# Optimization experiments

Measured on AMD Instinct MI355X. Metric: run time of the kernel, lower is better.

Reference implementation:

```python
import jax, jax.numpy as jnp
import numpy as np

TOP_K = 2


def setup_inputs() -> dict:
    key = jax.random.key(0)
    ks = jax.random.split(key, 10)
    D, F, E = 1024, 4096, 8
    s = 0.02  # realistic init scale, keeps activations stable
    return {
        "x": jax.random.normal(ks[0], (2, 4096, D), dtype=jnp.float32),
        "gate_w": jax.random.normal(ks[1], (E, D), dtype=jnp.float32) * s,
        "w1": jax.random.normal(ks[2], (E, F, D), dtype=jnp.float32) * s,
        "b1": jax.random.normal(ks[3], (E, F), dtype=jnp.float32) * s,
        "w2": jax.random.normal(ks[4], (E, D, F), dtype=jnp.float32) * s,
        "b2": jax.random.normal(ks[5], (E, D), dtype=jnp.float32) * s,
        "sw1": jax.random.normal(ks[6], (F, D), dtype=jnp.float32) * s,
        "sb1": jax.random.normal(ks[7], (F,), dtype=jnp.float32) * s,
        "sw2": jax.random.normal(ks[8], (D, F), dtype=jnp.float32) * s,
        "sb2": jax.random.normal(ks[9], (D,), dtype=jnp.float32) * s,
    }


def _ffn(x, w1, b1, w2, b2):
    # GELU(x @ W1^T + b1) @ W2^T + b2 ; torch F.gelu default = exact (erf)
    h = jax.nn.gelu(x @ w1.T + b1, approximate=False)
    return h @ w2.T + b2


def reference(x, gate_w, w1, b1, w2, b2, sw1, sb1, sw2, sb2):
    B, S, D = x.shape
    E = gate_w.shape[0]
    xt = x.reshape(-1, D)  # [T, D]

    # MoEGate: linear -> softmax -> top-k (weights not renormalized)
    scores = jax.nn.softmax(xt @ gate_w.T, axis=-1)  # [T, E]
    topk_w, topk_idx = jax.lax.top_k(scores, TOP_K)  # [T, K]

    # moe_infer: per-expert FFN, combine with top-k gate weights.
    # Reference form: dense per-expert compute, masked combine (combine sum is
    # permutation-invariant so top-k ordering does not matter).
    out = jnp.zeros_like(xt)
    for e in range(E):
        we = jnp.sum(jnp.where(topk_idx == e, topk_w, 0.0), axis=-1)  # [T]
        out = out + we[:, None] * _ffn(xt, w1[e], b1[e], w2[e], b2[e])

    # shared expert applied to the identity input
    out = out + _ffn(xt, sw1, sb1, sw2, sb2)
    return out.reshape(B, S, D)
```

## Files before the change

### kernel.cpp

```cpp
#include <hip/hip_runtime.h>
#include <hip/hip_bf16.h>

typedef __bf16 bf16_t;
typedef __bf16 bf16x4 __attribute__((ext_vector_type(4)));
typedef __bf16 bf16x8 __attribute__((ext_vector_type(8)));
typedef float  f32x4  __attribute__((ext_vector_type(4)));

static constexpr int TT = 8192;
static constexpr int DD = 1024;
static constexpr int FF = 4096;
static constexpr int NSLOT = 2 * TT;

#define R_COUNTS 0
#define R_OFFSET 8
#define R_TSTART 17
#define R_TOTAL  34
#define R_INTS   40

#define GLL(g, l) __builtin_amdgcn_global_load_lds( \
    (__attribute__((address_space(1))) void*)(g), \
    (__attribute__((address_space(3))) void*)(l), 16, 0, 0)

__device__ __forceinline__ float fast_gelu(float v) {
  float t = -1.5957691216f * v - 0.0713548162f * (v * v * v);
  return v / (1.f + __expf(t));
}

__global__ __launch_bounds__(256) void cvt_all(const float* __restrict__ w1,
                                               const float* __restrict__ w2,
                                               const float* __restrict__ sw1,
                                               const float* __restrict__ sw2,
                                               bf16_t* __restrict__ dst) {
  size_t i = (size_t)blockIdx.x * 256 + threadIdx.x;
  const float* src;
  size_t off;
  if (i < 4194304)      { src = w1;  off = i; }
  else if (i < 8388608) { src = w2;  off = i - 4194304; }
  else if (i < 8912896) { src = sw1; off = i - 8388608; }
  else                  { src = sw2; off = i - 8912896; }
  const float4* s = reinterpret_cast<const float4*>(src) + off * 2;
  float4 a = s[0], b = s[1];
  bf16x8 v;
  v[0] = (bf16_t)a.x; v[1] = (bf16_t)a.y; v[2] = (bf16_t)a.z; v[3] = (bf16_t)a.w;
  v[4] = (bf16_t)b.x; v[5] = (bf16_t)b.y; v[6] = (bf16_t)b.z; v[7] = (bf16_t)b.w;
  *reinterpret_cast<bf16x8*>(dst + i * 8) = v;
}

__global__ __launch_bounds__(256) void gate_kernel(const float* __restrict__ x,
                                                   const float* __restrict__ gw,
                                                   float* __restrict__ topkw,
                                                   int* __restrict__ slote,
                                                   bf16_t* __restrict__ xb) {
  int wid = threadIdx.x >> 6, lane = threadIdx.x & 63;
  int t = blockIdx.x * 4 + wid;
  const float4* xv = reinterpret_cast<const float4*>(x + (size_t)t * DD) + lane * 4;
  const float4* gv = reinterpret_cast<const float4*>(gw);
  float acc[8];
  float4 xs[4];
#pragma unroll
  for (int e = 0; e < 8; ++e) acc[e] = 0.f;
#pragma unroll
  for (int i = 0; i < 4; ++i) {
    float4 xi = xv[i];
    xs[i] = xi;
#pragma unroll
    for (int e = 0; e < 8; ++e) {
      float4 g = gv[e * 256 + lane * 4 + i];
      acc[e] += xi.x * g.x + xi.y * g.y + xi.z * g.z + xi.w * g.w;
    }
  }
  {
    bf16x8 lo, hi;
    lo[0]=(bf16_t)xs[0].x; lo[1]=(bf16_t)xs[0].y; lo[2]=(bf16_t)xs[0].z; lo[3]=(bf16_t)xs[0].w;
    lo[4]=(bf16_t)xs[1].x; lo[5]=(bf16_t)xs[1].y; lo[6]=(bf16_t)xs[1].z; lo[7]=(bf16_t)xs[1].w;
    hi[0]=(bf16_t)xs[2].x; hi[1]=(bf16_t)xs[2].y; hi[2]=(bf16_t)xs[2].z; hi[3]=(bf16_t)xs[2].w;
    hi[4]=(bf16_t)xs[3].x; hi[5]=(bf16_t)xs[3].y; hi[6]=(bf16_t)xs[3].z; hi[7]=(bf16_t)xs[3].w;
    bf16_t* d = xb + (size_t)t * DD + lane * 16;
    *reinterpret_cast<bf16x8*>(d) = lo;
    *reinterpret_cast<bf16x8*>(d + 8) = hi;
  }
#pragma unroll
  for (int e = 0; e < 8; ++e)
    for (int off = 32; off; off >>= 1) acc[e] += __shfl_xor(acc[e], off, 64);
  if (lane == 0) {
    float m = acc[0];
#pragma unroll
    for (int e = 1; e < 8; ++e) m = fmaxf(m, acc[e]);
    float p[8], s = 0.f;
#pragma unroll
    for (int e = 0; e < 8; ++e) { p[e] = expf(acc[e] - m); s += p[e]; }
    float inv = 1.f / s;
#pragma unroll
    for (int e = 0; e < 8; ++e) p[e] *= inv;
    int e1 = 0; float b1v = p[0];
#pragma unroll
    for (int e = 1; e < 8; ++e) if (p[e] > b1v) { b1v = p[e]; e1 = e; }
    int e2 = -1; float b2v = -1.f;
#pragma unroll
    for (int e = 0; e < 8; ++e) if (e != e1 && p[e] > b2v) { b2v = p[e]; e2 = e; }
    topkw[2 * t] = b1v;  topkw[2 * t + 1] = b2v;
    slote[2 * t] = e1;   slote[2 * t + 1] = e2;
  }
}

__global__ __launch_bounds__(256) void route_kernel(const int* __restrict__ slote,
                                                    int* __restrict__ routing,
                                                    int* __restrict__ perm,
                                                    int* __restrict__ pos) {
  __shared__ int sl[16384];
  __shared__ int red[256];
  __shared__ int wtot[4];
  const int e = blockIdx.x;
  const int t = threadIdx.x;
  const int lane = t & 63, wid = t >> 6;

  for (int i = t; i < NSLOT; i += 256) sl[i] = slote[i];
  __syncthreads();

  int cnt[8];
#pragma unroll
  for (int ee = 0; ee < 8; ++ee) cnt[ee] = 0;
  for (int i = t; i < NSLOT; i += 256) ++cnt[sl[i]];

  int tot[8];
#pragma unroll
  for (int ee = 0; ee < 8; ++ee) {
    red[t] = cnt[ee];
    __syncthreads();
    for (int s = 128; s; s >>= 1) {
      if (t < s) red[t] += red[t + s];
      __syncthreads();
    }
    tot[ee] = red[0];
    __syncthreads();
  }

  int offarr[9], tstart[9];
  {
    int off = 0, tts = 0;
#pragma unroll
    for (int ee = 0; ee < 8; ++ee) {
      offarr[ee] = off; tstart[ee] = tts;
      off += tot[ee]; tts += (tot[ee] + 127) >> 7;
    }
    offarr[8] = off; tstart[8] = tts;
  }
  if (e == 0 && t == 0) {
#pragma unroll
    for (int ee = 0; ee < 8; ++ee) routing[R_COUNTS + ee] = tot[ee];
#pragma unroll
    for (int ee = 0; ee < 9; ++ee) {
      routing[R_OFFSET + ee] = offarr[ee];
      routing[R_TSTART + ee] = tstart[ee];
    }
    routing[R_TOTAL] = tstart[8];
  }

  int running = offarr[e];
  for (int base = 0; base < NSLOT; base += 256) {
    int s = base + t;
    bool m = (sl[s] == e);
    unsigned long long mask = __ballot(m);
    int wrank = __popcll(mask & ((1ull << lane) - 1ull));
    if (lane == 0) wtot[wid] = __popcll(mask);
    __syncthreads();
    int wpre = 0;
#pragma unroll
    for (int w = 0; w < 4; ++w) if (w < wid) wpre += wtot[w];
    int totb = wtot[0] + wtot[1] + wtot[2] + wtot[3];
    if (m) {
      int pp = running + wpre + wrank;
      perm[pp] = s;
      pos[s] = pp;
    }
    running += totb;
    __syncthreads();
  }
}

template <int MODE>
__global__ __launch_bounds__(256, 4) void gemm_kernel(
    const bf16_t* __restrict__ A, const bf16_t* __restrict__ Bw,
    const float* __restrict__ bias, bf16_t* __restrict__ Hout,
    float* __restrict__ out, const int* __restrict__ routing,
    const int* __restrict__ perm, const float* __restrict__ topkw,
    const int* __restrict__ pos, const bf16_t* __restrict__ slotb) {
  constexpr bool EXPERT = (MODE < 2);
  constexpr int K = (MODE == 0 || MODE == 2) ? 1024 : 4096;
  constexpr int NTOT = (MODE == 0 || MODE == 2) ? 4096 : 1024;
  constexpr int NT = NTOT / 128;
  constexpr int NKT = K / 64;
  constexpr int OUTD = (MODE == 0 || MODE == 2) ? FF : DD;

  __shared__ __align__(16) bf16_t lds[16384];

  const int t = threadIdx.x;
  const int lane = t & 63;
  const int wid = t >> 6;
  const int wm = wid >> 1;
  const int wn = wid & 1;

  const int nwg = gridDim.x;
  const int q = nwg >> 3, r = nwg & 7;
  const int xcd = blockIdx.x & 7, bi = blockIdx.x >> 3;
  const int swz = (xcd < r ? xcd * (q + 1) : r * (q + 1) + (xcd - r) * q) + bi;
  const int mt = swz / NT;
  const int nt = swz & (NT - 1);

  int row0, valid, eidx = 0;
  if constexpr (EXPERT) {
    if (mt >= routing[R_TOTAL]) return;
    int e = 0;
    while (e < 7 && routing[R_TSTART + e + 1] <= mt) ++e;
    eidx = e;
    int lm = mt - routing[R_TSTART + e];
    row0 = routing[R_OFFSET + e] + lm * 128;
    valid = min(128, routing[R_COUNTS + e] - lm * 128);
  } else {
    row0 = mt * 128;
    valid = 128;
  }

  const bf16_t* Bexp = Bw + (EXPERT ? (size_t)eidx * NTOT * K : 0);
  const float* biasp = bias + (EXPERT ? eidx * NTOT : 0);

  const int sub = t >> 3;
  const int lc = (t & 7) ^ (sub & 7);
  const bf16_t* aS[4];
  const bf16_t* bS[4];
#pragma unroll
  for (int i = 0; i < 4; ++i) {
    int lr = sub + i * 32;
    int gr;
    if constexpr (MODE == 0) {
      gr = perm[row0 + min(lr, valid - 1)] >> 1;
    } else if constexpr (MODE == 1) {
      gr = row0 + min(lr, valid - 1);
    } else {
      gr = row0 + lr;
    }
    aS[i] = A + (size_t)gr * K + lc * 8;
    bS[i] = Bexp + (size_t)(nt * 128 + lr) * K + lc * 8;
  }
  bf16_t* const aD = lds + (sub << 6) + ((t & 7) << 3);
  bf16_t* const bD = aD + 8192;

  const int l15 = lane & 15, lq = lane >> 4;

  f32x4 acc[4][4];
#pragma unroll
  for (int m = 0; m < 4; ++m)
#pragma unroll
    for (int n = 0; n < 4; ++n) acc[m][n] = f32x4{0.f, 0.f, 0.f, 0.f};

  for (int kt = 0; kt < NKT; ++kt) {
    const size_t kof = (size_t)kt * 64;
#pragma unroll
    for (int i = 0; i < 4; ++i) {
      GLL(aS[i] + kof, aD + i * 2048);
      GLL(bS[i] + kof, bD + i * 2048);
    }
    __syncthreads();

#pragma unroll
    for (int kk = 0; kk < 2; ++kk) {
      bf16x8 af[4], bfr[4];
#pragma unroll
      for (int m = 0; m < 4; ++m) {
        int ra = wm * 64 + m * 16 + l15;
        int ph = (kk * 4 + lq) ^ (ra & 7);
        af[m] = *reinterpret_cast<const bf16x8*>(&lds[ra * 64 + ph * 8]);
      }
#pragma unroll
      for (int n = 0; n < 4; ++n) {
        int rb = wn * 64 + n * 16 + l15;
        int ph = (kk * 4 + lq) ^ (rb & 7);
        bfr[n] = *reinterpret_cast<const bf16x8*>(&lds[8192 + rb * 64 + ph * 8]);
      }
      __builtin_amdgcn_s_setprio(1);
#pragma unroll
      for (int m = 0; m < 4; ++m)
#pragma unroll
        for (int n = 0; n < 4; ++n)
          acc[m][n] = __builtin_amdgcn_mfma_f32_16x16x32_bf16(af[m], bfr[n], acc[m][n], 0, 0, 0);
      __builtin_amdgcn_s_setprio(0);
    }
    __syncthreads();
  }

  float bc[4];
#pragma unroll
  for (int n = 0; n < 4; ++n) bc[n] = biasp[nt * 128 + wn * 64 + n * 16 + l15];

  if constexpr (MODE != 3) {
    bf16_t* scr = lds;
#pragma unroll
    for (int h = 0; h < 2; ++h) {
      __syncthreads();
      if (wm == h) {
        float wsl[4][4];
        if constexpr (MODE == 1) {
#pragma unroll
          for (int m = 0; m < 4; ++m)
#pragma unroll
            for (int rr = 0; rr < 4; ++rr) {
              int lr = h * 64 + m * 16 + lq * 4 + rr;
              wsl[m][rr] = topkw[perm[row0 + min(lr, valid - 1)]];
            }
        }
#pragma unroll
        for (int m = 0; m < 4; ++m)
#pragma unroll
          for (int n = 0; n < 4; ++n)
#pragma unroll
            for (int rr = 0; rr < 4; ++rr) {
              float v = acc[m][n][rr] + bc[n];
              float o;
              if constexpr (MODE == 1) o = wsl[m][rr] * v;
              else                     o = fast_gelu(v);
              scr[(m * 16 + lq * 4 + rr) * 128 + wn * 64 + n * 16 + l15] = (bf16_t)o;
            }
      }
      __syncthreads();
#pragma unroll
      for (int i = 0; i < 4; ++i) {
        int c = t + i * 256;
        int rowp = c >> 4, cc = c & 15;
        int lr = h * 64 + rowp;
        if (lr < valid) {
          bf16x8 v8 = *reinterpret_cast<const bf16x8*>(&scr[rowp * 128 + cc * 8]);
          *reinterpret_cast<bf16x8*>(&Hout[(size_t)(row0 + lr) * OUTD + nt * 128 + cc * 8]) = v8;
        }
      }
    }
  } else {
    float* scr = reinterpret_cast<float*>(lds);
#pragma unroll
    for (int h = 0; h < 2; ++h) {
      __syncthreads();
      if (wm == h) {
#pragma unroll
        for (int m = 0; m < 4; ++m)
#pragma unroll
          for (int n = 0; n < 4; ++n)
#pragma unroll
            for (int rr = 0; rr < 4; ++rr)
              scr[(m * 16 + lq * 4 + rr) * 128 + wn * 64 + n * 16 + l15] = acc[m][n][rr] + bc[n];
      }
      __syncthreads();
#pragma unroll
      for (int i = 0; i < 8; ++i) {
        int c = t + i * 256;
        int rowp = c >> 5, cc = c & 31;
        int lr = h * 64 + rowp;
        int gp = row0 + lr;
        int p0 = pos[2 * gp], p1 = pos[2 * gp + 1];
        float4 v4 = *reinterpret_cast<const float4*>(&scr[rowp * 128 + cc * 4]);
        bf16x4 s0 = *reinterpret_cast<const bf16x4*>(&slotb[(size_t)p0 * DD + nt * 128 + cc * 4]);
        bf16x4 s1 = *reinterpret_cast<const bf16x4*>(&slotb[(size_t)p1 * DD + nt * 128 + cc * 4]);
        v4.x += (float)s0[0] + (float)s1[0];
        v4.y += (float)s0[1] + (float)s1[1];
        v4.z += (float)s0[2] + (float)s1[2];
        v4.w += (float)s0[3] + (float)s1[3];
        *reinterpret_cast<float4*>(&out[(size_t)gp * OUTD + nt * 128 + cc * 4]) = v4;
      }
    }
  }
}

extern "C" void kernel_launch(void* const* d_in, const int* in_sizes, int n_in,
                              void* d_out, int out_size, void* d_ws, size_t ws_size,
                              hipStream_t stream) {
  const float* x   = (const float*)d_in[0];
  const float* gw  = (const float*)d_in[1];
  const float* w1  = (const float*)d_in[2];
  const float* b1  = (const float*)d_in[3];
  const float* w2  = (const float*)d_in[4];
  const float* b2  = (const float*)d_in[5];
  const float* sw1 = (const float*)d_in[6];
  const float* sb1 = (const float*)d_in[7];
  const float* sw2 = (const float*)d_in[8];
  const float* sb2 = (const float*)d_in[9];
  float* out = (float*)d_out;

  char* ws = (char*)d_ws;
  bf16_t* xb    = (bf16_t*)(ws);
  bf16_t* w1b   = (bf16_t*)(ws + ((size_t)16 << 20));
  bf16_t* w2b   = (bf16_t*)(ws + ((size_t)80 << 20));
  bf16_t* sw1b  = (bf16_t*)(ws + ((size_t)144 << 20));
  bf16_t* sw2b  = (bf16_t*)(ws + ((size_t)152 << 20));
  bf16_t* Hbuf  = (bf16_t*)(ws + ((size_t)160 << 20));
  bf16_t* slotb = (bf16_t*)(ws + ((size_t)16 << 20));
  float*  topkw = (float*)(ws + ((size_t)288 << 20));
  int*    slote = (int*)(ws + ((size_t)288 << 20) + 65536);
  int*    perm  = (int*)(ws + ((size_t)288 << 20) + 2 * 65536);
  int*    pos   = (int*)(ws + ((size_t)288 << 20) + 3 * 65536);
  int*    routing = (int*)(ws + ((size_t)288 << 20) + 4 * 65536);

  cvt_all<<<9437184 / 256, 256, 0, stream>>>(w1, w2, sw1, sw2, w1b);

  gate_kernel<<<TT / 4, 256, 0, stream>>>(x, gw, topkw, slote, xb);
  route_kernel<<<8, 256, 0, stream>>>(slote, routing, perm, pos);

  gemm_kernel<0><<<136 * 32, 256, 0, stream>>>(xb, w1b, b1, Hbuf, nullptr, routing, perm, nullptr, nullptr, nullptr);
  gemm_kernel<1><<<136 * 8, 256, 0, stream>>>(Hbuf, w2b, b2, slotb, nullptr, routing, perm, topkw, nullptr, nullptr);
  gemm_kernel<2><<<64 * 32, 256, 0, stream>>>(xb, sw1b, sb1, Hbuf, nullptr, routing, perm, nullptr, nullptr, nullptr);
  gemm_kernel<3><<<64 * 8, 256, 0, stream>>>(Hbuf, sw2b, sb2, nullptr, out, routing, perm, nullptr, pos, slotb);
}
```

Measured before the change: 692.9 us.

## Merge weight conversion with gating and co-schedule expert GEMM2 with shared GEMM1

Weight fp32→bf16 conversion and the gate kernel now run as one launch, with the block index choosing the role. When the workspace is large enough, the expert down-projection GEMM and the shared-expert up-projection GEMM run as one grid. The shared hidden activations go to a separate buffer so the two GEMMs do not overwrite each other's inputs. This removes launch gaps and tail underutilization between independent stages, and it depends on the workspace size to enable the merged path.

```diff
diff --git a/kernel.cpp b/kernel.cpp
--- a/kernel.cpp
+++ b/kernel.cpp
@@ -10,6 +10,10 @@
 static constexpr int DD = 1024;
 static constexpr int FF = 4096;
 static constexpr int NSLOT = 2 * TT;
+static constexpr int GATE_BLKS = TT / 4;
+static constexpr int CVT_BLKS = 9437184 / 256;
+static constexpr int EG2_BLKS = 136 * 8;
+static constexpr int SG1_BLKS = 64 * 32;
 
 #define R_COUNTS 0
 #define R_OFFSET 8
@@ -26,31 +30,32 @@
   return v / (1.f + __expf(t));
 }
 
-__global__ __launch_bounds__(256) void cvt_all(const float* __restrict__ w1,
-                                               const float* __restrict__ w2,
-                                               const float* __restrict__ sw1,
-                                               const float* __restrict__ sw2,
-                                               bf16_t* __restrict__ dst) {
-  size_t i = (size_t)blockIdx.x * 256 + threadIdx.x;
-  const float* src;
-  size_t off;
-  if (i < 4194304)      { src = w1;  off = i; }
-  else if (i < 8388608) { src = w2;  off = i - 4194304; }
-  else if (i < 8912896) { src = sw1; off = i - 8388608; }
-  else                  { src = sw2; off = i - 8912896; }
-  const float4* s = reinterpret_cast<const float4*>(src) + off * 2;
-  float4 a = s[0], b = s[1];
-  bf16x8 v;
-  v[0] = (bf16_t)a.x; v[1] = (bf16_t)a.y; v[2] = (bf16_t)a.z; v[3] = (bf16_t)a.w;
-  v[4] = (bf16_t)b.x; v[5] = (bf16_t)b.y; v[6] = (bf16_t)b.z; v[7] = (bf16_t)b.w;
-  *reinterpret_cast<bf16x8*>(dst + i * 8) = v;
-}
-
-__global__ __launch_bounds__(256) void gate_kernel(const float* __restrict__ x,
+__global__ __launch_bounds__(256) void prep_kernel(const float* __restrict__ x,
                                                    const float* __restrict__ gw,
                                                    float* __restrict__ topkw,
                                                    int* __restrict__ slote,
-                                                   bf16_t* __restrict__ xb) {
+                                                   bf16_t* __restrict__ xb,
+                                                   const float* __restrict__ w1,
+                                                   const float* __restrict__ w2,
+                                                   const float* __restrict__ sw1,
+                                                   const float* __restrict__ sw2,
+                                                   bf16_t* __restrict__ wdst) {
+  if ((int)blockIdx.x >= GATE_BLKS) {
+    size_t i = (size_t)(blockIdx.x - GATE_BLKS) * 256 + threadIdx.x;
+    const float* src;
+    size_t off;
+    if (i < 4194304)      { src = w1;  off = i; }
+    else if (i < 8388608) { src = w2;  off = i - 4194304; }
+    else if (i < 8912896) { src = sw1; off = i - 8388608; }
+    else                  { src = sw2; off = i - 8912896; }
+    const float4* s = reinterpret_cast<const float4*>(src) + off * 2;
+    float4 a = s[0], b = s[1];
+    bf16x8 v;
+    v[0] = (bf16_t)a.x; v[1] = (bf16_t)a.y; v[2] = (bf16_t)a.z; v[3] = (bf16_t)a.w;
+    v[4] = (bf16_t)b.x; v[5] = (bf16_t)b.y; v[6] = (bf16_t)b.z; v[7] = (bf16_t)b.w;
+    *reinterpret_cast<bf16x8*>(wdst + i * 8) = v;
+    return;
+  }
   int wid = threadIdx.x >> 6, lane = threadIdx.x & 63;
   int t = blockIdx.x * 4 + wid;
   const float4* xv = reinterpret_cast<const float4*>(x + (size_t)t * DD) + lane * 4;
@@ -179,7 +184,8 @@
 }
 
 template <int MODE>
-__global__ __launch_bounds__(256, 4) void gemm_kernel(
+__device__ __forceinline__ void gemm_body(
+    int vbid, int nwg, bf16_t* lds,
     const bf16_t* __restrict__ A, const bf16_t* __restrict__ Bw,
     const float* __restrict__ bias, bf16_t* __restrict__ Hout,
     float* __restrict__ out, const int* __restrict__ routing,
@@ -192,17 +198,14 @@
   constexpr int NKT = K / 64;
   constexpr int OUTD = (MODE == 0 || MODE == 2) ? FF : DD;
 
-  __shared__ __align__(16) bf16_t lds[16384];
-
   const int t = threadIdx.x;
   const int lane = t & 63;
   const int wid = t >> 6;
   const int wm = wid >> 1;
   const int wn = wid & 1;
 
-  const int nwg = gridDim.x;
   const int q = nwg >> 3, r = nwg & 7;
-  const int xcd = blockIdx.x & 7, bi = blockIdx.x >> 3;
+  const int xcd = vbid & 7, bi = vbid >> 3;
   const int swz = (xcd < r ? xcd * (q + 1) : r * (q + 1) + (xcd - r) * q) + bi;
   const int mt = swz / NT;
   const int nt = swz & (NT - 1);
@@ -368,6 +371,35 @@
   }
 }
 
+template <int MODE>
+__global__ __launch_bounds__(256, 4) void gemm_single(
+    const bf16_t* __restrict__ A, const bf16_t* __restrict__ Bw,
+    const float* __restrict__ bias, bf16_t* __restrict__ Hout,
+    float* __restrict__ out, const int* __restrict__ routing,
+    const int* __restrict__ perm, const float* __restrict__ topkw,
+    const int* __restrict__ pos, const bf16_t* __restrict__ slotb) {
+  __shared__ __align__(16) bf16_t lds[16384];
+  gemm_body<MODE>(blockIdx.x, gridDim.x, lds, A, Bw, bias, Hout, out,
+                  routing, perm, topkw, pos, slotb);
+}
+
+__global__ __launch_bounds__(256, 4) void gemm_eg2_sg1(
+    const bf16_t* __restrict__ Hexp, const bf16_t* __restrict__ w2b,
+    const float* __restrict__ b2, bf16_t* __restrict__ slotb,
+    const bf16_t* __restrict__ xb, const bf16_t* __restrict__ sw1b,
+    const float* __restrict__ sb1, bf16_t* __restrict__ sHbuf,
+    const int* __restrict__ routing, const int* __restrict__ perm,
+    const float* __restrict__ topkw) {
+  __shared__ __align__(16) bf16_t lds[16384];
+  if ((int)blockIdx.x < EG2_BLKS) {
+    gemm_body<1>(blockIdx.x, EG2_BLKS, lds, Hexp, w2b, b2, slotb, nullptr,
+                 routing, perm, topkw, nullptr, nullptr);
+  } else {
+    gemm_body<2>(blockIdx.x - EG2_BLKS, SG1_BLKS, lds, xb, sw1b, sb1, sHbuf,
+                 nullptr, routing, perm, nullptr, nullptr, nullptr);
+  }
+}
+
 extern "C" void kernel_launch(void* const* d_in, const int* in_sizes, int n_in,
                               void* d_out, int out_size, void* d_ws, size_t ws_size,
                               hipStream_t stream) {
@@ -397,13 +429,25 @@
   int*    pos   = (int*)(ws + ((size_t)288 << 20) + 3 * 65536);
   int*    routing = (int*)(ws + ((size_t)288 << 20) + 4 * 65536);
 
-  cvt_all<<<9437184 / 256, 256, 0, stream>>>(w1, w2, sw1, sw2, w1b);
-
-  gate_kernel<<<TT / 4, 256, 0, stream>>>(x, gw, topkw, slote, xb);
+  const bool bigws = ws_size >= ((size_t)368 << 20);
+  bf16_t* sHbuf = bigws ? (bf16_t*)(ws + ((size_t)304 << 20)) : Hbuf;
+
+  prep_kernel<<<GATE_BLKS + CVT_BLKS, 256, 0, stream>>>(x, gw, topkw, slote, xb,
+                                                        w1, w2, sw1, sw2, w1b);
   route_kernel<<<8, 256, 0, stream>>>(slote, routing, perm, pos);
 
-  gemm_kernel<0><<<136 * 32, 256, 0, stream>>>(xb, w1b, b1, Hbuf, nullptr, routing, perm, nullptr, nullptr, nullptr);
-  gemm_kernel<1><<<136 * 8, 256, 0, stream>>>(Hbuf, w2b, b2, slotb, nullptr, routing, perm, topkw, nullptr, nullptr);
-  gemm_kernel<2><<<64 * 32, 256, 0, stream>>>(xb, sw1b, sb1, Hbuf, nullptr, routing, perm, nullptr, nullptr, nullptr);
-  gemm_kernel<3><<<64 * 8, 256, 0, stream>>>(Hbuf, sw2b, sb2, nullptr, out, routing, perm, nullptr, pos, slotb);
-}
+  gemm_single<0><<<136 * 32, 256, 0, stream>>>(xb, w1b, b1, Hbuf, nullptr, routing,
+                                               perm, nullptr, nullptr, nullptr);
+  if (bigws) {
+    gemm_eg2_sg1<<<EG2_BLKS + SG1_BLKS, 256, 0, stream>>>(Hbuf, w2b, b2, slotb,
+                                                          xb, sw1b, sb1, sHbuf,
+                                                          routing, perm, topkw);
+  } else {
+    gemm_single<1><<<EG2_BLKS, 256, 0, stream>>>(Hbuf, w2b, b2, slotb, nullptr,
+                                                 routing, perm, topkw, nullptr, nullptr);
+    gemm_single<2><<<SG1_BLKS, 256, 0, stream>>>(xb, sw1b, sb1, Hbuf, nullptr,
+                                                 routing, perm, nullptr, nullptr, nullptr);
+  }
+  gemm_single<3><<<64 * 8, 256, 0, stream>>>(sHbuf, sw2b, sb2, nullptr, out, routing,
+                                             perm, nullptr, pos, slotb);
+}
```

After: 632.8 us, median of 2. -8.7%, faster.
